# Performance work log

Measured on AMD Instinct MI355X. Metric: run time of the kernel, lower is better.

Reference implementation:

```python
import jax, jax.numpy as jnp
import numpy as np

WINDOW_SIZE = 11
SIGMA = 1.5
C2 = 0.03 ** 2

_KX = np.array([[-1, 0, 1], [-2, 0, 2], [-1, 0, 1]], dtype=np.float32)
_KY = np.array([[1, 2, 1], [0, 0, 0], [-1, -2, -1]], dtype=np.float32)


def _gaussian_window(channel):
    xs = np.arange(WINDOW_SIZE) - WINDOW_SIZE // 2
    g = np.exp(-(xs.astype(np.float64) ** 2) / (2.0 * SIGMA ** 2))
    g = (g / g.sum()).astype(np.float32)
    w2 = np.outer(g, g)  # [11,11]
    return jnp.asarray(np.tile(w2[None, None], (channel, 1, 1, 1)))  # [C,1,11,11]


def _dwconv(x, k, pad):
    # depthwise NCHW conv, groups = channels
    return jax.lax.conv_general_dilated(
        x, k, window_strides=(1, 1), padding=[(pad, pad), (pad, pad)],
        feature_group_count=x.shape[1],
        dimension_numbers=("NCHW", "OIHW", "NCHW"))


def _sobel_grad(x):
    c = x.shape[1]
    kx = jnp.asarray(np.tile(_KX[None, None], (c, 1, 1, 1)))
    ky = jnp.asarray(np.tile(_KY[None, None], (c, 1, 1, 1)))
    return jnp.abs(_dwconv(x, kx, 1)) + jnp.abs(_dwconv(x, ky, 1))


def _ssim(img1, img2, img3):
    # img1 = generated, img2 = ir, img3 = vis (matches torch call order)
    c = img1.shape[1]
    w = _gaussian_window(c)
    pad = WINDOW_SIZE // 2
    conv = lambda t: _dwconv(t, w, pad)
    mu1, mu2, mu3 = conv(img1), conv(img2), conv(img3)
    sigma1_sq = conv(img1 * img1) - mu1 * mu1
    sigma2_sq = conv(img2 * img2) - mu2 * mu2
    sigma3_sq = conv(img3 * img3) - mu3 * mu3
    sigma12 = conv(img1 * img2) - mu1 * mu2
    sigma13 = conv(img1 * img3) - mu1 * mu3
    x2 = jnp.sqrt(sigma2_sq)
    x3 = jnp.sqrt(sigma3_sq)
    ssim_map_12 = (2 * sigma12 + C2) / (sigma1_sq + sigma2_sq + C2)
    ssim_map_13 = (2 * sigma13 + C2) / (sigma1_sq + sigma3_sq + C2)
    ssim_map_std = jnp.where(jnp.abs(x2) >= jnp.abs(x3), ssim_map_12, ssim_map_13)
    return ssim_map_std.mean()


def setup_inputs() -> dict:
    key = jax.random.key(0)
    k1, k2, k3 = jax.random.split(key, 3)
    shape = (32, 1, 512, 512)
    return {
        "vis": jax.random.uniform(k1, shape, dtype=jnp.float32),
        "ir": jax.random.uniform(k2, shape, dtype=jnp.float32),
        "generate_img": jax.random.uniform(k3, shape, dtype=jnp.float32),
    }


def reference(vis, ir, generate_img):
    # intensity loss: L1 against pixel-wise max of vis/ir
    x_in_max = jnp.maximum(vis, ir)
    loss_in = 1.5 * jnp.mean(jnp.abs(generate_img - x_in_max))
    # gradient loss: L1 between sobel magnitude of fused image and joint max gradient
    y_grad = _sobel_grad(vis)
    ir_grad = _sobel_grad(ir)
    gen_grad = _sobel_grad(generate_img)
    x_grad_joint = jnp.maximum(y_grad, ir_grad)
    loss_grad = jnp.mean(jnp.abs(gen_grad - x_grad_joint))
    lssim = 0.5 * (1.0 - _ssim(generate_img, ir, vis))
    return (loss_in, lssim + loss_grad)
```

## Files before the change

### kernel.cpp

```cpp
#include <hip/hip_runtime.h>

#define NB 32
#define W 512
#define H 512
#define BLOCK 512
#define BAND 32
#define RS 4
#define NSTEP (BAND / RS)
#define PADW 524
#define C2f 0.0009f

#define GW0 0.001028381f
#define GW1 0.007598758f
#define GW2 0.036000773f
#define GW3 0.109360700f
#define GW4 0.213005540f
#define GW5 0.266011720f

__device__ __forceinline__ float gwv(int k) {
    const float g[11] = {GW0, GW1, GW2, GW3, GW4, GW5, GW4, GW3, GW2, GW1, GW0};
    return g[k];
}

template<bool GY>
__device__ __forceinline__ float ldy(const float* __restrict__ p, int gy, int col) {
    if (GY) {
        bool ok = (unsigned)gy < H;
        int cy = min(max(gy, 0), H - 1);
        float v = p[cy * W + col];
        return ok ? v : 0.f;
    }
    return p[gy * W + col];
}

template<bool GY>
__device__ __forceinline__ float ldxy(const float* __restrict__ p, int gy, int gx) {
    int cx = min(max(gx, 0), W - 1);
    if (GY) {
        bool ok = ((unsigned)gx < W) && ((unsigned)gy < H);
        int cy = min(max(gy, 0), H - 1);
        float v = p[cy * W + cx];
        return ok ? v : 0.f;
    }
    float v = p[gy * W + cx];
    return ((unsigned)gx < W) ? v : 0.f;
}

__device__ __forceinline__ float sob3(const float r0[3], const float r1[3],
                                      const float r2[3]) {
    float gx = (r0[2] - r0[0]) + 2.f * (r1[2] - r1[0]) + (r2[2] - r2[0]);
    float gy = (r0[0] - r2[0]) + 2.f * (r0[1] - r2[1]) + (r0[2] - r2[2]);
    return fabsf(gx) + fabsf(gy);
}

template<bool GY>
__device__ __forceinline__ void vstep(
    const float* __restrict__ pg, const float* __restrict__ pi,
    const float* __restrict__ pv, float* __restrict__ vsf,
    int rbase, int col) {
    float acc[RS][8];
    #pragma unroll
    for (int j = 0; j < RS; ++j)
        #pragma unroll
        for (int q = 0; q < 8; ++q) acc[j][q] = 0.f;

    #pragma unroll
    for (int k = 0; k < RS + 10; ++k) {
        int gy = rbase - 5 + k;
        float a = ldy<GY>(pg, gy, col);
        float b = ldy<GY>(pi, gy, col);
        float c = ldy<GY>(pv, gy, col);
        float aa = a * a, bb = b * b, cc = c * c, ab = a * b, ac = a * c;
        #pragma unroll
        for (int j = 0; j < RS; ++j) {
            int t = k - j;
            if (t >= 0 && t <= 10) {
                float w = gwv(t);
                acc[j][0] = fmaf(w, a,  acc[j][0]);
                acc[j][1] = fmaf(w, b,  acc[j][1]);
                acc[j][2] = fmaf(w, c,  acc[j][2]);
                acc[j][3] = fmaf(w, aa, acc[j][3]);
                acc[j][4] = fmaf(w, bb, acc[j][4]);
                acc[j][5] = fmaf(w, cc, acc[j][5]);
                acc[j][6] = fmaf(w, ab, acc[j][6]);
                acc[j][7] = fmaf(w, ac, acc[j][7]);
            }
        }
    }
    #pragma unroll
    for (int j = 0; j < RS; ++j)
        #pragma unroll
        for (int q = 0; q < 8; ++q)
            vsf[(q * RS + j) * PADW + 5 + col] = acc[j][q];
}

template<bool GY>
__device__ __forceinline__ void sobstep(
    const float* __restrict__ pg, const float* __restrict__ pi,
    const float* __restrict__ pv, int rbase, int col,
    float& s_in, float& s_grad) {
    float g0[3], g1[3], g2[3], i0[3], i1[3], i2[3], v0[3], v1[3], v2[3];
    #pragma unroll
    for (int c = 0; c < 3; ++c) {
        int gx = col - 1 + c;
        g0[c] = ldxy<GY>(pg, rbase - 1, gx);
        i0[c] = ldxy<GY>(pi, rbase - 1, gx);
        v0[c] = ldxy<GY>(pv, rbase - 1, gx);
        g1[c] = ldxy<GY>(pg, rbase, gx);
        i1[c] = ldxy<GY>(pi, rbase, gx);
        v1[c] = ldxy<GY>(pv, rbase, gx);
    }
    #pragma unroll
    for (int j = 0; j < RS; ++j) {
        int gy = rbase + 1 + j;
        #pragma unroll
        for (int c = 0; c < 3; ++c) {
            int gx = col - 1 + c;
            g2[c] = ldxy<GY>(pg, gy, gx);
            i2[c] = ldxy<GY>(pi, gy, gx);
            v2[c] = ldxy<GY>(pv, gy, gx);
        }
        s_in += fabsf(g1[1] - fmaxf(v1[1], i1[1]));
        float sg = sob3(g0, g1, g2);
        float si = sob3(i0, i1, i2);
        float sv = sob3(v0, v1, v2);
        s_grad += fabsf(sg - fmaxf(sv, si));
        #pragma unroll
        for (int c = 0; c < 3; ++c) {
            g0[c] = g1[c]; g1[c] = g2[c];
            i0[c] = i1[c]; i1[c] = i2[c];
            v0[c] = v1[c]; v1[c] = v2[c];
        }
    }
}

__device__ __forceinline__ void hstep(const float* __restrict__ vsf, int tid,
                                      float& s_ssim) {
    int r = tid & 3;
    int xb = (tid >> 2) << 2;
    float res[8][4];
    #pragma unroll
    for (int q = 0; q < 8; ++q) {
        const float4* rp =
            reinterpret_cast<const float4*>(vsf + (q * RS + r) * PADW + xb);
        float4 A = rp[0], B = rp[1], C = rp[2], D = rp[3];
        float w[16] = {A.x, A.y, A.z, A.w, B.x, B.y, B.z, B.w,
                       C.x, C.y, C.z, C.w, D.x, D.y, D.z, D.w};
        #pragma unroll
        for (int j = 0; j < 4; ++j) {
            float acc = 0.f;
            #pragma unroll
            for (int t = 0; t < 11; ++t) acc = fmaf(gwv(t), w[j + t], acc);
            res[q][j] = acc;
        }
    }
    #pragma unroll
    for (int j = 0; j < 4; ++j) {
        float m1 = res[0][j], m2 = res[1][j], m3 = res[2][j];
        float sig1 = res[3][j] - m1 * m1;
        float sig2 = res[4][j] - m2 * m2;
        float sig3 = res[5][j] - m3 * m3;
        float sg12 = res[6][j] - m1 * m2;
        float sg13 = res[7][j] - m1 * m3;
        float x2 = sqrtf(sig2);
        float x3 = sqrtf(sig3);
        float map12 = (2.f * sg12 + C2f) / (sig1 + sig2 + C2f);
        float map13 = (2.f * sg13 + C2f) / (sig1 + sig3 + C2f);
        s_ssim += (fabsf(x2) >= fabsf(x3)) ? map12 : map13;
    }
}

__global__ __launch_bounds__(BLOCK)
__attribute__((amdgpu_waves_per_eu(4, 4))) void fusion_main(
    const float* __restrict__ vis, const float* __restrict__ ir,
    const float* __restrict__ gen, double* __restrict__ sums) {
    __shared__ float vsf[8 * RS * PADW];
    __shared__ float red[3][8];
    const size_t off = (size_t)blockIdx.z * (H * W);
    const int y0 = blockIdx.y * BAND;
    const int tid = threadIdx.x;
    const float* pv = vis + off;
    const float* pi = ir + off;
    const float* pg = gen + off;

    if (tid < 8 * RS * 12) {
        int plane = tid / 12;
        int rem = tid - plane * 12;
        int idx = (rem < 5) ? rem : (512 + rem);
        vsf[plane * PADW + idx] = 0.f;
    }
    __syncthreads();

    float s_in = 0.f, s_grad = 0.f, s_ssim = 0.f;
    bool interior = (blockIdx.y >= 1) && (blockIdx.y <= (H / BAND) - 2);

    if (interior) {
        for (int s = 0; s < NSTEP; ++s) {
            int rbase = y0 + s * RS;
            vstep<false>(pg, pi, pv, vsf, rbase, tid);
            __syncthreads();
            sobstep<false>(pg, pi, pv, rbase, tid, s_in, s_grad);
            hstep(vsf, tid, s_ssim);
            __syncthreads();
        }
    } else {
        for (int s = 0; s < NSTEP; ++s) {
            int rbase = y0 + s * RS;
            vstep<true>(pg, pi, pv, vsf, rbase, tid);
            __syncthreads();
            sobstep<true>(pg, pi, pv, rbase, tid, s_in, s_grad);
            hstep(vsf, tid, s_ssim);
            __syncthreads();
        }
    }

    #pragma unroll
    for (int o = 32; o > 0; o >>= 1) {
        s_in   += __shfl_down(s_in, o);
        s_grad += __shfl_down(s_grad, o);
        s_ssim += __shfl_down(s_ssim, o);
    }
    int lane = tid & 63, wv = tid >> 6;
    if (lane == 0) { red[0][wv] = s_in; red[1][wv] = s_grad; red[2][wv] = s_ssim; }
    __syncthreads();
    if (tid == 0) {
        float a = 0.f, b = 0.f, c = 0.f;
        #pragma unroll
        for (int k = 0; k < 8; ++k) { a += red[0][k]; b += red[1][k]; c += red[2][k]; }
        atomicAdd(&sums[0], (double)a);
        atomicAdd(&sums[1], (double)b);
        atomicAdd(&sums[2], (double)c);
    }
}

__global__ void finalize(const double* __restrict__ sums, float* __restrict__ out) {
    const double inv = 1.0 / ((double)NB * H * W);
    out[0] = (float)(1.5 * sums[0] * inv);
    out[1] = (float)(0.5 * (1.0 - sums[2] * inv) + sums[1] * inv);
}

extern "C" void kernel_launch(void* const* d_in, const int* in_sizes, int n_in,
                              void* d_out, int out_size, void* d_ws, size_t ws_size,
                              hipStream_t stream) {
    const float* vis = (const float*)d_in[0];
    const float* ir  = (const float*)d_in[1];
    const float* gen = (const float*)d_in[2];
    float* out = (float*)d_out;
    double* sums = (double*)d_ws;

    hipMemsetAsync(d_ws, 0, 3 * sizeof(double), stream);
    dim3 grid(1, H / BAND, NB);
    fusion_main<<<grid, BLOCK, 0, stream>>>(vis, ir, gen, sums);
    finalize<<<1, 1, 0, stream>>>(sums, out);
}
```

Measured before the change: 194.5 us.

## Halve shared staging buffer via two-pass horizontal filter and raise occupancy

The 8 vertically filtered planes now go through shared memory in two halves of 4. Each half gets its own horizontal pass, and the SSIM combine runs after both. This halves LDS use per block, the band height drops from 32 to 16 rows to launch more blocks, and the waves-per-EU hint goes from a fixed 4 to a minimum of 8. The trade-off is an extra pair of barriers per step, more overlapping halo rows recomputed per band, and register pressure from holding all 32 accumulators plus the first-half results.

New measurement: 366.0 us. +88.2%, slower.

```diff
diff --git a/kernel.cpp b/kernel.cpp
--- a/kernel.cpp
+++ b/kernel.cpp
@@ -4,10 +4,11 @@
 #define W 512
 #define H 512
 #define BLOCK 512
-#define BAND 32
+#define BAND 16
 #define RS 4
 #define NSTEP (BAND / RS)
 #define PADW 524
+#define NPL 4
 #define C2f 0.0009f
 
 #define GW0 0.001028381f
@@ -54,11 +55,9 @@
 }
 
 template<bool GY>
-__device__ __forceinline__ void vstep(
+__device__ __forceinline__ void vcompute(
     const float* __restrict__ pg, const float* __restrict__ pi,
-    const float* __restrict__ pv, float* __restrict__ vsf,
-    int rbase, int col) {
-    float acc[RS][8];
+    const float* __restrict__ pv, int rbase, int col, float (&acc)[RS][8]) {
     #pragma unroll
     for (int j = 0; j < RS; ++j)
         #pragma unroll
@@ -87,11 +86,6 @@
             }
         }
     }
-    #pragma unroll
-    for (int j = 0; j < RS; ++j)
-        #pragma unroll
-        for (int q = 0; q < 8; ++q)
-            vsf[(q * RS + j) * PADW + 5 + col] = acc[j][q];
 }
 
 template<bool GY>
@@ -134,13 +128,12 @@
     }
 }
 
-__device__ __forceinline__ void hstep(const float* __restrict__ vsf, int tid,
-                                      float& s_ssim) {
+__device__ __forceinline__ void hstep4(const float* __restrict__ vsf, int tid,
+                                       float (&res)[NPL][4]) {
     int r = tid & 3;
     int xb = (tid >> 2) << 2;
-    float res[8][4];
-    #pragma unroll
-    for (int q = 0; q < 8; ++q) {
+    #pragma unroll
+    for (int q = 0; q < NPL; ++q) {
         const float4* rp =
             reinterpret_cast<const float4*>(vsf + (q * RS + r) * PADW + xb);
         float4 A = rp[0], B = rp[1], C = rp[2], D = rp[3];
@@ -154,14 +147,19 @@
             res[q][j] = acc;
         }
     }
+}
+
+__device__ __forceinline__ void ssim_final(const float (&ra)[NPL][4],
+                                           const float (&rb)[NPL][4],
+                                           float& s_ssim) {
     #pragma unroll
     for (int j = 0; j < 4; ++j) {
-        float m1 = res[0][j], m2 = res[1][j], m3 = res[2][j];
-        float sig1 = res[3][j] - m1 * m1;
-        float sig2 = res[4][j] - m2 * m2;
-        float sig3 = res[5][j] - m3 * m3;
-        float sg12 = res[6][j] - m1 * m2;
-        float sg13 = res[7][j] - m1 * m3;
+        float m1 = ra[0][j], m2 = ra[1][j], m3 = ra[2][j];
+        float sig1 = ra[3][j] - m1 * m1;
+        float sig2 = rb[0][j] - m2 * m2;
+        float sig3 = rb[1][j] - m3 * m3;
+        float sg12 = rb[2][j] - m1 * m2;
+        float sg13 = rb[3][j] - m1 * m3;
         float x2 = sqrtf(sig2);
         float x3 = sqrtf(sig3);
         float map12 = (2.f * sg12 + C2f) / (sig1 + sig2 + C2f);
@@ -170,11 +168,40 @@
     }
 }
 
+template<bool GY>
+__device__ __forceinline__ void do_step(
+    const float* __restrict__ pg, const float* __restrict__ pi,
+    const float* __restrict__ pv, float* __restrict__ vsf,
+    int rbase, int tid, float& s_in, float& s_grad, float& s_ssim) {
+    float acc[RS][8];
+    vcompute<GY>(pg, pi, pv, rbase, tid, acc);
+    #pragma unroll
+    for (int j = 0; j < RS; ++j)
+        #pragma unroll
+        for (int q = 0; q < NPL; ++q)
+            vsf[(q * RS + j) * PADW + 5 + tid] = acc[j][q];
+    __syncthreads();
+    sobstep<GY>(pg, pi, pv, rbase, tid, s_in, s_grad);
+    float resA[NPL][4];
+    hstep4(vsf, tid, resA);
+    __syncthreads();
+    #pragma unroll
+    for (int j = 0; j < RS; ++j)
+        #pragma unroll
+        for (int q = 0; q < NPL; ++q)
+            vsf[(q * RS + j) * PADW + 5 + tid] = acc[j][q + NPL];
+    __syncthreads();
+    float resB[NPL][4];
+    hstep4(vsf, tid, resB);
+    ssim_final(resA, resB, s_ssim);
+    __syncthreads();
+}
+
 __global__ __launch_bounds__(BLOCK)
-__attribute__((amdgpu_waves_per_eu(4, 4))) void fusion_main(
+__attribute__((amdgpu_waves_per_eu(8))) void fusion_main(
     const float* __restrict__ vis, const float* __restrict__ ir,
     const float* __restrict__ gen, double* __restrict__ sums) {
-    __shared__ float vsf[8 * RS * PADW];
+    __shared__ float vsf[NPL * RS * PADW];
     __shared__ float red[3][8];
     const size_t off = (size_t)blockIdx.z * (H * W);
     const int y0 = blockIdx.y * BAND;
@@ -183,7 +210,7 @@
     const float* pi = ir + off;
     const float* pg = gen + off;
 
-    if (tid < 8 * RS * 12) {
+    if (tid < NPL * RS * 12) {
         int plane = tid / 12;
         int rem = tid - plane * 12;
         int idx = (rem < 5) ? rem : (512 + rem);
@@ -195,23 +222,13 @@
     bool interior = (blockIdx.y >= 1) && (blockIdx.y <= (H / BAND) - 2);
 
     if (interior) {
-        for (int s = 0; s < NSTEP; ++s) {
-            int rbase = y0 + s * RS;
-            vstep<false>(pg, pi, pv, vsf, rbase, tid);
-            __syncthreads();
-            sobstep<false>(pg, pi, pv, rbase, tid, s_in, s_grad);
-            hstep(vsf, tid, s_ssim);
-            __syncthreads();
-        }
+        for (int s = 0; s < NSTEP; ++s)
+            do_step<false>(pg, pi, pv, vsf, y0 + s * RS, tid,
+                           s_in, s_grad, s_ssim);
     } else {
-        for (int s = 0; s < NSTEP; ++s) {
-            int rbase = y0 + s * RS;
-            vstep<true>(pg, pi, pv, vsf, rbase, tid);
-            __syncthreads();
-            sobstep<true>(pg, pi, pv, rbase, tid, s_in, s_grad);
-            hstep(vsf, tid, s_ssim);
-            __syncthreads();
-        }
+        for (int s = 0; s < NSTEP; ++s)
+            do_step<true>(pg, pi, pv, vsf, y0 + s * RS, tid,
+                          s_in, s_grad, s_ssim);
     }
 
     #pragma unroll
```
